# Optimization experiments

Measured on AMD Instinct MI355X. Metric: run time of the kernel, lower is better.

Reference implementation:

```python
import jax, jax.numpy as jnp
import numpy as np

N = 16384
H = 2048
E = 8
I_PER_E = 8192 // E  # expert_intermediate_size = 1024


def setup_inputs() -> dict:
    key = jax.random.key(0)
    k1, k2, k3, k4 = jax.random.split(key, 4)
    hidden_states = jax.random.normal(k1, (N, H), dtype=jnp.float32)
    # sort_idx is a permutation of [0, N): tokens sorted by expert assignment
    sort_idx = jax.random.permutation(k2, N).astype(jnp.int64)
    # kaiming_uniform_ with a=sqrt(5): bound = sqrt(6/((1+a^2)*fan_in)) = 1/sqrt(fan_in)
    bound = 1.0 / np.sqrt(H)
    gate_up_proj = jax.random.uniform(k3, (E, H, 2 * I_PER_E), dtype=jnp.float32,
                                      minval=-bound, maxval=bound)
    # original inits down_proj to zeros; use small random so backward is non-trivial
    down_proj = jax.random.normal(k4, (E, I_PER_E, H), dtype=jnp.float32) * 0.02
    return {"hidden_states": hidden_states, "sort_idx": sort_idx,
            "gate_up_proj": gate_up_proj, "down_proj": down_proj}


def reference(hidden_states, sort_idx, gate_up_proj, down_proj):
    n, h = hidden_states.shape
    e = gate_up_proj.shape[0]
    chunk = n // e
    # gather tokens into expert order: [E, chunk, H]
    sorted_x = hidden_states[sort_idx].reshape(e, chunk, h)
    # fused gate+up grouped GEMM: [E, chunk, 2*I/E]
    gu = jnp.einsum('ech,ehf->ecf', sorted_x, gate_up_proj)
    gate, up = jnp.split(gu, 2, axis=-1)
    activated = jax.nn.silu(gate) * up  # [E, chunk, I/E]
    sorted_out = jnp.einsum('eci,eih->ech', activated, down_proj).reshape(n, h)
    # scatter back: out[sort_idx] = sorted_out
    out = jnp.zeros((n, h), dtype=sorted_out.dtype).at[sort_idx].set(sorted_out)
    return out
```

## Files before the change

### kernel.cpp

```cpp
#include <hip/hip_runtime.h>
#include <hip/hip_bf16.h>

#define N_TOK 16384
#define H_DIM 2048
#define NE 8
#define CHUNK 2048
#define IPE 1024
#define F2 2048

typedef __bf16 bf16;
typedef bf16 bf16x8 __attribute__((ext_vector_type(8)));
typedef float f32x4 __attribute__((ext_vector_type(4)));

typedef __attribute__((address_space(1))) void gvoid;
typedef __attribute__((address_space(3))) void svoid;

__device__ __forceinline__ void gload_lds16(const void* g, void* l) {
  __builtin_amdgcn_global_load_lds((gvoid*)g, (svoid*)l, 16, 0, 0);
}
__device__ __forceinline__ f32x4 MF(bf16x8 a, bf16x8 b, f32x4 c) {
  return __builtin_amdgcn_mfma_f32_16x16x32_bf16(a, b, c, 0, 0, 0);
}

#define BAR() __builtin_amdgcn_s_barrier()
#define LGKM0() asm volatile("s_waitcnt lgkmcnt(0)" ::: "memory")
#define LGKM8() asm volatile("s_waitcnt lgkmcnt(8)" ::: "memory")
#define VM6() asm volatile("s_waitcnt vmcnt(6)" ::: "memory")
#define VM0() asm volatile("s_waitcnt vmcnt(0)" ::: "memory")
#define PRIO(x) __builtin_amdgcn_s_setprio(x)
#define SCHED0() __builtin_amdgcn_sched_barrier(0)

__global__ __launch_bounds__(256) void k_gather(
    const float* __restrict__ x, const int* __restrict__ sidx,
    bf16* __restrict__ xs) {
  int row = blockIdx.x;
  int src = sidx[row];
  const float4* ip = (const float4*)(x + (size_t)src * H_DIM);
  int t = threadIdx.x;
  float4 f0 = ip[t * 2], f1 = ip[t * 2 + 1];
  bf16x8 v;
  v[0] = (bf16)f0.x; v[1] = (bf16)f0.y; v[2] = (bf16)f0.z; v[3] = (bf16)f0.w;
  v[4] = (bf16)f1.x; v[5] = (bf16)f1.y; v[6] = (bf16)f1.z; v[7] = (bf16)f1.w;
  *(bf16x8*)(xs + (size_t)row * H_DIM + t * 8) = v;
}

__global__ __launch_bounds__(256) void k_tr_w1(const float* __restrict__ in,
                                               bf16* __restrict__ out) {
  int e = blockIdx.z;
  int fB = blockIdx.x;
  int hB = blockIdx.y;
  __shared__ bf16 lds[64][68];
  int tx = threadIdx.x & 63;
  int ty = threadIdx.x >> 6;
  const float* ip = in + ((size_t)e * H_DIM + hB * 64) * F2;
  int scol = (tx < 32) ? (fB * 32 + tx) : (1024 + fB * 32 + (tx - 32));
#pragma unroll
  for (int p = 0; p < 16; ++p) {
    int hl = p * 4 + ty;
    lds[hl][tx] = (bf16)ip[(size_t)hl * F2 + scol];
  }
  __syncthreads();
  bf16* op = out + ((size_t)e * F2 + fB * 64) * H_DIM + hB * 64;
#pragma unroll
  for (int p = 0; p < 16; ++p) {
    int fl = p * 4 + ty;
    int g = fl >> 4, w = fl & 15;
    int lcol = ((g >> 1) << 4) + w + ((g & 1) << 5);
    op[(size_t)fl * H_DIM + tx] = lds[tx][lcol];
  }
}

__global__ __launch_bounds__(256) void k_tr_w2(const float* __restrict__ in,
                                               bf16* __restrict__ out) {
  int e = blockIdx.z;
  int hB = blockIdx.x;
  int iB = blockIdx.y;
  __shared__ bf16 lds[64][68];
  int tx = threadIdx.x & 63;
  int ty = threadIdx.x >> 6;
  const float* ip = in + (size_t)e * IPE * H_DIM + (size_t)iB * 64 * H_DIM + hB * 64;
#pragma unroll
  for (int p = 0; p < 16; ++p) {
    int il = p * 4 + ty;
    lds[il][tx] = (bf16)ip[(size_t)il * H_DIM + tx];
  }
  __syncthreads();
  bf16* op = out + (size_t)e * H_DIM * IPE + (size_t)hB * 64 * IPE + iB * 64;
#pragma unroll
  for (int p = 0; p < 16; ++p) {
    int hl = p * 4 + ty;
    op[(size_t)hl * IPE + tx] = lds[tx][hl];
  }
}

template <int KDIM, bool SILU>
__global__ __launch_bounds__(512, 2) void k_gemm8(
    const bf16* __restrict__ Aptr, const bf16* __restrict__ Bptr,
    const int* __restrict__ sidx, bf16* __restrict__ act,
    float* __restrict__ fout) {
  extern __shared__ char smem[];
  const int tid = threadIdx.x, lane = tid & 63, wv = tid >> 6;
  const int wm = wv >> 2, wn = wv & 3;
  constexpr int NT = KDIM / 64;

  int swzwg = (blockIdx.x & 7) * (gridDim.x >> 3) + (blockIdx.x >> 3);
  const int e = swzwg >> 6, bm = (swzwg >> 3) & 7, bn = swzwg & 7;

  const char* Ab = (const char*)(Aptr + ((size_t)e * CHUNK + bm * 256) * KDIM);
  const char* Bb = (const char*)(Bptr + ((size_t)e * 2048 + bn * 256) * KDIM);

  const int L0 = wv * 1024 + lane * 16;
  const int lin0 = L0 ^ (((L0 >> 7) & 7) << 4);
  const int srow0 = lin0 >> 7, scolb = lin0 & 127;

  const int rA = lane & 15;
  const int swzr = (rA & 7) << 4;
  const int cb = (lane >> 4) * 16;

  f32x4 acc[8][4] = {};

  auto stage = [&](int buf, int mat, int half, int kt) {
    const char* gb = (mat == 0) ? Ab : Bb;
    char* ld = smem + buf * 65536 + mat * 32768 + half * 16384 + wv * 1024;
    size_t rb = (size_t)(half * 128 + srow0) * (KDIM * 2) + (size_t)kt * 128 + scolb;
    gload_lds16(gb + rb, ld);
    gload_lds16(gb + rb + (size_t)64 * (KDIM * 2), ld + 8192);
  };
  auto ldA = [&](int buf, int mi, int ks) {
    int lin = ((mi * 16 + rA) << 7) + ks * 64 + cb;
    return *(const bf16x8*)(smem + buf * 65536 + wm * 16384 + (lin ^ swzr));
  };
  auto ldB = [&](int buf, int ni, int ks) {
    int lin = (((wn & 1) * 64 + ni * 16 + rA) << 7) + ks * 64 + cb;
    return *(const bf16x8*)(smem + buf * 65536 + 32768 + (wn >> 1) * 16384 + (lin ^ swzr));
  };

  stage(0, 1, 0, 0); stage(0, 1, 1, 0); stage(0, 0, 0, 0); stage(0, 0, 1, 0);
  stage(1, 1, 0, 1); stage(1, 1, 1, 1); stage(1, 0, 0, 1);
  VM6();
  BAR();

  auto ktile = [&](int t, int cur) {
    const int nxt = cur ^ 1;
    bf16x8 AA[4][2], B0[2][2], B1[2][2];
#pragma unroll
    for (int mi = 0; mi < 4; ++mi) {
      AA[mi][0] = ldA(cur, mi, 0);
      AA[mi][1] = ldA(cur, mi, 1);
    }
#pragma unroll
    for (int ni = 0; ni < 2; ++ni) {
      B0[ni][0] = ldB(cur, ni, 0);
      B0[ni][1] = ldB(cur, ni, 1);
    }
    if (t + 1 < NT) stage(nxt, 0, 1, t + 1);
    LGKM8();
    BAR();
    LGKM0();
    SCHED0();
    PRIO(1);
#pragma unroll
    for (int mi = 0; mi < 4; ++mi)
#pragma unroll
      for (int ni = 0; ni < 2; ++ni) {
        acc[mi][ni] = MF(AA[mi][0], B0[ni][0], acc[mi][ni]);
        acc[mi][ni] = MF(AA[mi][1], B0[ni][1], acc[mi][ni]);
      }
    PRIO(0);
    BAR();
#pragma unroll
    for (int ni = 0; ni < 2; ++ni) {
      B1[ni][0] = ldB(cur, 2 + ni, 0);
      B1[ni][1] = ldB(cur, 2 + ni, 1);
    }
    if (t + 2 < NT) stage(cur, 1, 0, t + 2);
    BAR();
    LGKM0();
    SCHED0();
    PRIO(1);
#pragma unroll
    for (int mi = 0; mi < 4; ++mi)
#pragma unroll
      for (int ni = 0; ni < 2; ++ni) {
        acc[mi][2 + ni] = MF(AA[mi][0], B1[ni][0], acc[mi][2 + ni]);
        acc[mi][2 + ni] = MF(AA[mi][1], B1[ni][1], acc[mi][2 + ni]);
      }
    PRIO(0);
    BAR();
#pragma unroll
    for (int mi = 0; mi < 4; ++mi) {
      AA[mi][0] = ldA(cur, 4 + mi, 0);
      AA[mi][1] = ldA(cur, 4 + mi, 1);
    }
    if (t + 2 < NT) stage(cur, 1, 1, t + 2);
    BAR();
    LGKM0();
    SCHED0();
    PRIO(1);
#pragma unroll
    for (int mi = 0; mi < 4; ++mi)
#pragma unroll
      for (int ni = 0; ni < 2; ++ni) {
        acc[4 + mi][ni] = MF(AA[mi][0], B0[ni][0], acc[4 + mi][ni]);
        acc[4 + mi][ni] = MF(AA[mi][1], B0[ni][1], acc[4 + mi][ni]);
      }
    PRIO(0);
    BAR();
    if (t + 2 < NT) {
      stage(cur, 0, 0, t + 2);
      VM6();
    } else if (t + 1 < NT) {
      VM0();
    }
    BAR();
    PRIO(1);
#pragma unroll
    for (int mi = 0; mi < 4; ++mi)
#pragma unroll
      for (int ni = 0; ni < 2; ++ni) {
        acc[4 + mi][2 + ni] = MF(AA[mi][0], B1[ni][0], acc[4 + mi][2 + ni]);
        acc[4 + mi][2 + ni] = MF(AA[mi][1], B1[ni][1], acc[4 + mi][2 + ni]);
      }
    PRIO(0);
    BAR();
  };

  for (int tt = 0; tt < NT; tt += 2) {
    ktile(tt, 0);
    ktile(tt + 1, 1);
  }

  if constexpr (SILU) {
    bf16* actp = act + ((size_t)e * CHUNK + bm * 256 + wm * 128) * IPE;
    const int r0 = (lane >> 4) * 4;
    const int c0 = bn * 128 + wn * 32 + (lane & 15);
#pragma unroll
    for (int mi = 0; mi < 8; ++mi)
#pragma unroll
      for (int p = 0; p < 2; ++p) {
        f32x4 g = acc[mi][2 * p], u = acc[mi][2 * p + 1];
#pragma unroll
        for (int r = 0; r < 4; ++r) {
          float gv = g[r];
          float a = gv / (1.f + __expf(-gv)) * u[r];
          actp[(size_t)(mi * 16 + r0 + r) * IPE + c0 + p * 16] = (bf16)a;
        }
      }
  } else {
    const int* sp = sidx + e * CHUNK + bm * 256 + wm * 128;
    const int r0 = (lane >> 4) * 4;
    const int c0 = bn * 256 + wn * 64 + (lane & 15);
#pragma unroll
    for (int mi = 0; mi < 8; ++mi)
#pragma unroll
      for (int r = 0; r < 4; ++r) {
        int dst = sp[mi * 16 + r0 + r];
        float* op = fout + (size_t)dst * H_DIM + c0;
#pragma unroll
        for (int ni = 0; ni < 4; ++ni) op[ni * 16] = acc[mi][ni][r];
      }
  }
}

extern "C" void kernel_launch(void* const* d_in, const int* in_sizes, int n_in,
                              void* d_out, int out_size, void* d_ws, size_t ws_size,
                              hipStream_t stream) {
  const float* hidden = (const float*)d_in[0];
  const int* sidx = (const int*)d_in[1];
  const float* w1 = (const float*)d_in[2];
  const float* w2 = (const float*)d_in[3];
  float* out = (float*)d_out;

  char* ws = (char*)d_ws;
  bf16* xs  = (bf16*)(ws);
  bf16* w1t = (bf16*)(ws + (size_t)67108864);
  bf16* act = (bf16*)(ws + (size_t)134217728);
  bf16* w2t = (bf16*)(ws);

  hipFuncSetAttribute((const void*)k_gemm8<H_DIM, true>,
                      hipFuncAttributeMaxDynamicSharedMemorySize, 131072);
  hipFuncSetAttribute((const void*)k_gemm8<IPE, false>,
                      hipFuncAttributeMaxDynamicSharedMemorySize, 131072);

  k_gather<<<dim3(N_TOK), 256, 0, stream>>>(hidden, sidx, xs);
  k_tr_w1<<<dim3(32, 32, NE), 256, 0, stream>>>(w1, w1t);
  k_gemm8<H_DIM, true><<<dim3(512), 512, 131072, stream>>>(xs, w1t, nullptr, act, nullptr);
  k_tr_w2<<<dim3(32, 16, NE), 256, 0, stream>>>(w2, w2t);
  k_gemm8<IPE, false><<<dim3(512), 512, 131072, stream>>>(act, w2t, sidx, nullptr, out);
}
```

Before: 307.0 us.

## Fuse gather and weight transpose/convert into GEMM prologue loads

Removes the separate gather, w1 transpose and w2 transpose kernels. The first GEMM now reads fp32 hidden rows through sort_idx and fp32 w1 columns directly, converts them to bf16 in registers, and writes them into swizzled LDS. The second GEMM does the same for w2. This drops three launches and the workspace round-trips, at the cost of strided scalar fp32 weight loads, more register pressure, and a weaker software pipeline with a full vmcnt(0) wait each tile. The weight conversion is also repeated by every block that shares a weight tile, instead of being done once.

Result: slower. 1.172 ms (+281.9%).

```diff
diff --git a/kernel.cpp b/kernel.cpp
--- a/kernel.cpp
+++ b/kernel.cpp
@@ -25,106 +25,71 @@
 #define BAR() __builtin_amdgcn_s_barrier()
 #define LGKM0() asm volatile("s_waitcnt lgkmcnt(0)" ::: "memory")
 #define LGKM8() asm volatile("s_waitcnt lgkmcnt(8)" ::: "memory")
-#define VM6() asm volatile("s_waitcnt vmcnt(6)" ::: "memory")
 #define VM0() asm volatile("s_waitcnt vmcnt(0)" ::: "memory")
 #define PRIO(x) __builtin_amdgcn_s_setprio(x)
 #define SCHED0() __builtin_amdgcn_sched_barrier(0)
 
-__global__ __launch_bounds__(256) void k_gather(
-    const float* __restrict__ x, const int* __restrict__ sidx,
-    bf16* __restrict__ xs) {
-  int row = blockIdx.x;
-  int src = sidx[row];
-  const float4* ip = (const float4*)(x + (size_t)src * H_DIM);
-  int t = threadIdx.x;
-  float4 f0 = ip[t * 2], f1 = ip[t * 2 + 1];
-  bf16x8 v;
-  v[0] = (bf16)f0.x; v[1] = (bf16)f0.y; v[2] = (bf16)f0.z; v[3] = (bf16)f0.w;
-  v[4] = (bf16)f1.x; v[5] = (bf16)f1.y; v[6] = (bf16)f1.z; v[7] = (bf16)f1.w;
-  *(bf16x8*)(xs + (size_t)row * H_DIM + t * 8) = v;
-}
-
-__global__ __launch_bounds__(256) void k_tr_w1(const float* __restrict__ in,
-                                               bf16* __restrict__ out) {
-  int e = blockIdx.z;
-  int fB = blockIdx.x;
-  int hB = blockIdx.y;
-  __shared__ bf16 lds[64][68];
-  int tx = threadIdx.x & 63;
-  int ty = threadIdx.x >> 6;
-  const float* ip = in + ((size_t)e * H_DIM + hB * 64) * F2;
-  int scol = (tx < 32) ? (fB * 32 + tx) : (1024 + fB * 32 + (tx - 32));
-#pragma unroll
-  for (int p = 0; p < 16; ++p) {
-    int hl = p * 4 + ty;
-    lds[hl][tx] = (bf16)ip[(size_t)hl * F2 + scol];
-  }
-  __syncthreads();
-  bf16* op = out + ((size_t)e * F2 + fB * 64) * H_DIM + hB * 64;
-#pragma unroll
-  for (int p = 0; p < 16; ++p) {
-    int fl = p * 4 + ty;
-    int g = fl >> 4, w = fl & 15;
-    int lcol = ((g >> 1) << 4) + w + ((g & 1) << 5);
-    op[(size_t)fl * H_DIM + tx] = lds[tx][lcol];
-  }
-}
-
-__global__ __launch_bounds__(256) void k_tr_w2(const float* __restrict__ in,
-                                               bf16* __restrict__ out) {
-  int e = blockIdx.z;
-  int hB = blockIdx.x;
-  int iB = blockIdx.y;
-  __shared__ bf16 lds[64][68];
-  int tx = threadIdx.x & 63;
-  int ty = threadIdx.x >> 6;
-  const float* ip = in + (size_t)e * IPE * H_DIM + (size_t)iB * 64 * H_DIM + hB * 64;
-#pragma unroll
-  for (int p = 0; p < 16; ++p) {
-    int il = p * 4 + ty;
-    lds[il][tx] = (bf16)ip[(size_t)il * H_DIM + tx];
-  }
-  __syncthreads();
-  bf16* op = out + (size_t)e * H_DIM * IPE + (size_t)hB * 64 * IPE + iB * 64;
-#pragma unroll
-  for (int p = 0; p < 16; ++p) {
-    int hl = p * 4 + ty;
-    op[(size_t)hl * IPE + tx] = lds[tx][hl];
-  }
-}
-
-template <int KDIM, bool SILU>
-__global__ __launch_bounds__(512, 2) void k_gemm8(
-    const bf16* __restrict__ Aptr, const bf16* __restrict__ Bptr,
-    const int* __restrict__ sidx, bf16* __restrict__ act,
-    float* __restrict__ fout) {
+__global__ __launch_bounds__(512, 2) void k_mlp1(
+    const float* __restrict__ hidden, const int* __restrict__ sidx,
+    const float* __restrict__ w1, bf16* __restrict__ act) {
   extern __shared__ char smem[];
   const int tid = threadIdx.x, lane = tid & 63, wv = tid >> 6;
   const int wm = wv >> 2, wn = wv & 3;
-  constexpr int NT = KDIM / 64;
-
-  int swzwg = (blockIdx.x & 7) * (gridDim.x >> 3) + (blockIdx.x >> 3);
-  const int e = swzwg >> 6, bm = (swzwg >> 3) & 7, bn = swzwg & 7;
-
-  const char* Ab = (const char*)(Aptr + ((size_t)e * CHUNK + bm * 256) * KDIM);
-  const char* Bb = (const char*)(Bptr + ((size_t)e * 2048 + bn * 256) * KDIM);
-
-  const int L0 = wv * 1024 + lane * 16;
-  const int lin0 = L0 ^ (((L0 >> 7) & 7) << 4);
-  const int srow0 = lin0 >> 7, scolb = lin0 & 127;
+  constexpr int NT = H_DIM / 64;
+
+  const int orig = blockIdx.x;
+  const int e = orig >> 6, bm = (orig >> 3) & 7, bn = orig & 7;
+
+  const int mA = tid >> 1;
+  const int khalf = (tid & 1) * 32;
+  const int srcTok = sidx[e * CHUNK + bm * 256 + mA];
+  const float* Arow = hidden + (size_t)srcTok * H_DIM + khalf;
+  const int AwOff = ((mA >> 7) << 14) + ((mA & 127) << 7);
+  const int swzA = (mA & 7) << 4;
+
+  const int np = tid >> 1;
+  const int fcol = bn * 128 + ((np >> 6) & 3) * 32 + ((np >> 5) & 1) * 16 +
+                   (np & 15) + ((np >> 4) & 1) * 1024;
+  const float* Bcol = w1 + (size_t)e * H_DIM * F2 + fcol;
+  const int BwOff = 32768 + ((np >> 7) << 14) + ((np & 127) << 7);
+  const int swzB = (np & 7) << 4;
 
   const int rA = lane & 15;
   const int swzr = (rA & 7) << 4;
   const int cb = (lane >> 4) * 16;
 
   f32x4 acc[8][4] = {};
-
-  auto stage = [&](int buf, int mat, int half, int kt) {
-    const char* gb = (mat == 0) ? Ab : Bb;
-    char* ld = smem + buf * 65536 + mat * 32768 + half * 16384 + wv * 1024;
-    size_t rb = (size_t)(half * 128 + srow0) * (KDIM * 2) + (size_t)kt * 128 + scolb;
-    gload_lds16(gb + rb, ld);
-    gload_lds16(gb + rb + (size_t)64 * (KDIM * 2), ld + 8192);
+  float4 aload[8];
+  float bl[32];
+
+  auto issueA = [&](int kbase) {
+#pragma unroll
+    for (int j = 0; j < 8; ++j)
+      aload[j] = *(const float4*)(Arow + kbase + j * 4);
+  };
+  auto writeA = [&](int buf) {
+#pragma unroll
+    for (int w = 0; w < 4; ++w) {
+      float4 u0 = aload[2 * w], u1 = aload[2 * w + 1];
+      bf16x8 tv;
+      tv[0] = (bf16)u0.x; tv[1] = (bf16)u0.y; tv[2] = (bf16)u0.z; tv[3] = (bf16)u0.w;
+      tv[4] = (bf16)u1.x; tv[5] = (bf16)u1.y; tv[6] = (bf16)u1.z; tv[7] = (bf16)u1.w;
+      *(bf16x8*)(smem + buf * 65536 + AwOff + ((khalf * 2 + w * 16) ^ swzA)) = tv;
+    }
+  };
+  auto issueB = [&](int kbase) {
+    const float* bp = Bcol + (size_t)(kbase + khalf) * F2;
+#pragma unroll
+    for (int j = 0; j < 32; ++j) bl[j] = bp[(size_t)j * F2];
+  };
+  auto writeB = [&](int buf) {
+#pragma unroll
+    for (int w = 0; w < 4; ++w) {
+      bf16x8 tv;
+#pragma unroll
+      for (int i = 0; i < 8; ++i) tv[i] = (bf16)bl[w * 8 + i];
+      *(bf16x8*)(smem + buf * 65536 + BwOff + ((khalf * 2 + w * 16) ^ swzB)) = tv;
+    }
   };
   auto ldA = [&](int buf, int mi, int ks) {
     int lin = ((mi * 16 + rA) << 7) + ks * 64 + cb;
@@ -135,9 +100,12 @@
     return *(const bf16x8*)(smem + buf * 65536 + 32768 + (wn >> 1) * 16384 + (lin ^ swzr));
   };
 
-  stage(0, 1, 0, 0); stage(0, 1, 1, 0); stage(0, 0, 0, 0); stage(0, 0, 1, 0);
-  stage(1, 1, 0, 1); stage(1, 1, 1, 1); stage(1, 0, 0, 1);
-  VM6();
+  issueA(0);
+  issueB(0);
+  writeA(0);
+  writeB(0);
+  issueA(64);
+  LGKM0();
   BAR();
 
   auto ktile = [&](int t, int cur) {
@@ -153,7 +121,6 @@
       B0[ni][0] = ldB(cur, ni, 0);
       B0[ni][1] = ldB(cur, ni, 1);
     }
-    if (t + 1 < NT) stage(nxt, 0, 1, t + 1);
     LGKM8();
     BAR();
     LGKM0();
@@ -173,7 +140,7 @@
       B1[ni][0] = ldB(cur, 2 + ni, 0);
       B1[ni][1] = ldB(cur, 2 + ni, 1);
     }
-    if (t + 2 < NT) stage(cur, 1, 0, t + 2);
+    if (t + 1 < NT) writeA(nxt);
     BAR();
     LGKM0();
     SCHED0();
@@ -192,7 +159,7 @@
       AA[mi][0] = ldA(cur, 4 + mi, 0);
       AA[mi][1] = ldA(cur, 4 + mi, 1);
     }
-    if (t + 2 < NT) stage(cur, 1, 1, t + 2);
+    if (t + 1 < NT) issueB((t + 1) * 64);
     BAR();
     LGKM0();
     SCHED0();
@@ -206,12 +173,9 @@
       }
     PRIO(0);
     BAR();
-    if (t + 2 < NT) {
-      stage(cur, 0, 0, t + 2);
-      VM6();
-    } else if (t + 1 < NT) {
-      VM0();
-    }
+    if (t + 1 < NT) writeB(nxt);
+    if (t + 2 < NT) issueA((t + 2) * 64);
+    LGKM0();
     BAR();
     PRIO(1);
 #pragma unroll
@@ -230,36 +194,192 @@
     ktile(tt + 1, 1);
   }
 
-  if constexpr (SILU) {
-    bf16* actp = act + ((size_t)e * CHUNK + bm * 256 + wm * 128) * IPE;
-    const int r0 = (lane >> 4) * 4;
-    const int c0 = bn * 128 + wn * 32 + (lane & 15);
-#pragma unroll
-    for (int mi = 0; mi < 8; ++mi)
-#pragma unroll
-      for (int p = 0; p < 2; ++p) {
-        f32x4 g = acc[mi][2 * p], u = acc[mi][2 * p + 1];
-#pragma unroll
-        for (int r = 0; r < 4; ++r) {
-          float gv = g[r];
-          float a = gv / (1.f + __expf(-gv)) * u[r];
-          actp[(size_t)(mi * 16 + r0 + r) * IPE + c0 + p * 16] = (bf16)a;
-        }
-      }
-  } else {
-    const int* sp = sidx + e * CHUNK + bm * 256 + wm * 128;
-    const int r0 = (lane >> 4) * 4;
-    const int c0 = bn * 256 + wn * 64 + (lane & 15);
-#pragma unroll
-    for (int mi = 0; mi < 8; ++mi)
+  bf16* actp = act + ((size_t)e * CHUNK + bm * 256 + wm * 128) * IPE;
+  const int r0 = (lane >> 4) * 4;
+  const int c0 = bn * 128 + wn * 32 + (lane & 15);
+#pragma unroll
+  for (int mi = 0; mi < 8; ++mi)
+#pragma unroll
+    for (int p = 0; p < 2; ++p) {
+      f32x4 g = acc[mi][2 * p], u = acc[mi][2 * p + 1];
 #pragma unroll
       for (int r = 0; r < 4; ++r) {
-        int dst = sp[mi * 16 + r0 + r];
-        float* op = fout + (size_t)dst * H_DIM + c0;
-#pragma unroll
-        for (int ni = 0; ni < 4; ++ni) op[ni * 16] = acc[mi][ni][r];
-      }
+        float gv = g[r];
+        float a = gv / (1.f + __expf(-gv)) * u[r];
+        actp[(size_t)(mi * 16 + r0 + r) * IPE + c0 + p * 16] = (bf16)a;
+      }
+    }
+}
+
+__global__ __launch_bounds__(512, 2) void k_mlp2(
+    const bf16* __restrict__ act, const float* __restrict__ w2,
+    const int* __restrict__ sidx, float* __restrict__ out) {
+  extern __shared__ char smem[];
+  const int tid = threadIdx.x, lane = tid & 63, wv = tid >> 6;
+  const int wm = wv >> 2, wn = wv & 3;
+  constexpr int NT = IPE / 64;
+
+  const int orig = blockIdx.x;
+  const int e = orig >> 6, bm = (orig >> 3) & 7, bn = orig & 7;
+
+  const char* Ab = (const char*)(act + ((size_t)e * CHUNK + bm * 256) * IPE);
+
+  const int L0 = wv * 1024 + lane * 16;
+  const int lin0 = L0 ^ (((L0 >> 7) & 7) << 4);
+  const int srow0 = lin0 >> 7, scolb = lin0 & 127;
+
+  const int np = tid >> 1;
+  const int khalf = (tid & 1) * 32;
+  const float* Bcol = w2 + (size_t)e * IPE * H_DIM + bn * 256 + np;
+  const int BwOff = 32768 + ((np >> 7) << 14) + ((np & 127) << 7);
+  const int swzB = (np & 7) << 4;
+
+  const int rA = lane & 15;
+  const int swzr = (rA & 7) << 4;
+  const int cb = (lane >> 4) * 16;
+
+  f32x4 acc[8][4] = {};
+  float bl[32];
+
+  auto stageA = [&](int buf, int kt) {
+#pragma unroll
+    for (int half = 0; half < 2; ++half) {
+      char* ld = smem + buf * 65536 + half * 16384 + wv * 1024;
+      size_t rb = (size_t)(half * 128 + srow0) * (IPE * 2) + (size_t)kt * 128 + scolb;
+      gload_lds16(Ab + rb, ld);
+      gload_lds16(Ab + rb + (size_t)64 * (IPE * 2), ld + 8192);
+    }
+  };
+  auto issueB = [&](int kbase) {
+    const float* bp = Bcol + (size_t)(kbase + khalf) * H_DIM;
+#pragma unroll
+    for (int j = 0; j < 32; ++j) bl[j] = bp[(size_t)j * H_DIM];
+  };
+  auto writeB = [&](int buf) {
+#pragma unroll
+    for (int w = 0; w < 4; ++w) {
+      bf16x8 tv;
+#pragma unroll
+      for (int i = 0; i < 8; ++i) tv[i] = (bf16)bl[w * 8 + i];
+      *(bf16x8*)(smem + buf * 65536 + BwOff + ((khalf * 2 + w * 16) ^ swzB)) = tv;
+    }
+  };
+  auto ldA = [&](int buf, int mi, int ks) {
+    int lin = ((mi * 16 + rA) << 7) + ks * 64 + cb;
+    return *(const bf16x8*)(smem + buf * 65536 + wm * 16384 + (lin ^ swzr));
+  };
+  auto ldB = [&](int buf, int ni, int ks) {
+    int lin = (((wn & 1) * 64 + ni * 16 + rA) << 7) + ks * 64 + cb;
+    return *(const bf16x8*)(smem + buf * 65536 + 32768 + (wn >> 1) * 16384 + (lin ^ swzr));
+  };
+
+  stageA(0, 0);
+  issueB(0);
+  writeB(0);
+  VM0();
+  LGKM0();
+  BAR();
+
+  auto ktile = [&](int t, int cur) {
+    const int nxt = cur ^ 1;
+    bf16x8 AA[4][2], B0[2][2], B1[2][2];
+#pragma unroll
+    for (int mi = 0; mi < 4; ++mi) {
+      AA[mi][0] = ldA(cur, mi, 0);
+      AA[mi][1] = ldA(cur, mi, 1);
+    }
+#pragma unroll
+    for (int ni = 0; ni < 2; ++ni) {
+      B0[ni][0] = ldB(cur, ni, 0);
+      B0[ni][1] = ldB(cur, ni, 1);
+    }
+    if (t + 1 < NT) stageA(nxt, t + 1);
+    LGKM8();
+    BAR();
+    LGKM0();
+    SCHED0();
+    PRIO(1);
+#pragma unroll
+    for (int mi = 0; mi < 4; ++mi)
+#pragma unroll
+      for (int ni = 0; ni < 2; ++ni) {
+        acc[mi][ni] = MF(AA[mi][0], B0[ni][0], acc[mi][ni]);
+        acc[mi][ni] = MF(AA[mi][1], B0[ni][1], acc[mi][ni]);
+      }
+    PRIO(0);
+    BAR();
+#pragma unroll
+    for (int ni = 0; ni < 2; ++ni) {
+      B1[ni][0] = ldB(cur, 2 + ni, 0);
+      B1[ni][1] = ldB(cur, 2 + ni, 1);
+    }
+    BAR();
+    LGKM0();
+    SCHED0();
+    PRIO(1);
+#pragma unroll
+    for (int mi = 0; mi < 4; ++mi)
+#pragma unroll
+      for (int ni = 0; ni < 2; ++ni) {
+        acc[mi][2 + ni] = MF(AA[mi][0], B1[ni][0], acc[mi][2 + ni]);
+        acc[mi][2 + ni] = MF(AA[mi][1], B1[ni][1], acc[mi][2 + ni]);
+      }
+    PRIO(0);
+    BAR();
+#pragma unroll
+    for (int mi = 0; mi < 4; ++mi) {
+      AA[mi][0] = ldA(cur, 4 + mi, 0);
+      AA[mi][1] = ldA(cur, 4 + mi, 1);
+    }
+    if (t + 1 < NT) issueB((t + 1) * 64);
+    BAR();
+    LGKM0();
+    SCHED0();
+    PRIO(1);
+#pragma unroll
+    for (int mi = 0; mi < 4; ++mi)
+#pragma unroll
+      for (int ni = 0; ni < 2; ++ni) {
+        acc[4 + mi][ni] = MF(AA[mi][0], B0[ni][0], acc[4 + mi][ni]);
+        acc[4 + mi][ni] = MF(AA[mi][1], B0[ni][1], acc[4 + mi][ni]);
+      }
+    PRIO(0);
+    BAR();
+    if (t + 1 < NT) {
+      writeB(nxt);
+      VM0();
+    }
+    LGKM0();
+    BAR();
+    PRIO(1);
+#pragma unroll
+    for (int mi = 0; mi < 4; ++mi)
+#pragma unroll
+      for (int ni = 0; ni < 2; ++ni) {
+        acc[4 + mi][2 + ni] = MF(AA[mi][0], B1[ni][0], acc[4 + mi][2 + ni]);
+        acc[4 + mi][2 + ni] = MF(AA[mi][1], B1[ni][1], acc[4 + mi][2 + ni]);
+      }
+    PRIO(0);
+    BAR();
+  };
+
+  for (int tt = 0; tt < NT; tt += 2) {
+    ktile(tt, 0);
+    ktile(tt + 1, 1);
   }
+
+  const int* sp = sidx + e * CHUNK + bm * 256 + wm * 128;
+  const int r0 = (lane >> 4) * 4;
+  const int c0 = bn * 256 + wn * 64 + (lane & 15);
+#pragma unroll
+  for (int mi = 0; mi < 8; ++mi)
+#pragma unroll
+    for (int r = 0; r < 4; ++r) {
+      int dst = sp[mi * 16 + r0 + r];
+      float* op = out + (size_t)dst * H_DIM + c0;
+#pragma unroll
+      for (int ni = 0; ni < 4; ++ni) op[ni * 16] = acc[mi][ni][r];
+    }
 }
 
 extern "C" void kernel_launch(void* const* d_in, const int* in_sizes, int n_in,
@@ -271,20 +391,13 @@
   const float* w2 = (const float*)d_in[3];
   float* out = (float*)d_out;
 
-  char* ws = (char*)d_ws;
-  bf16* xs  = (bf16*)(ws);
-  bf16* w1t = (bf16*)(ws + (size_t)67108864);
-  bf16* act = (bf16*)(ws + (size_t)134217728);
-  bf16* w2t = (bf16*)(ws);
-
-  hipFuncSetAttribute((const void*)k_gemm8<H_DIM, true>,
+  bf16* act = (bf16*)d_ws;
+
+  hipFuncSetAttribute((const void*)k_mlp1,
                       hipFuncAttributeMaxDynamicSharedMemorySize, 131072);
-  hipFuncSetAttribute((const void*)k_gemm8<IPE, false>,
+  hipFuncSetAttribute((const void*)k_mlp2,
                       hipFuncAttributeMaxDynamicSharedMemorySize, 131072);
 
-  k_gather<<<dim3(N_TOK), 256, 0, stream>>>(hidden, sidx, xs);
-  k_tr_w1<<<dim3(32, 32, NE), 256, 0, stream>>>(w1, w1t);
-  k_gemm8<H_DIM, true><<<dim3(512), 512, 131072, stream>>>(xs, w1t, nullptr, act, nullptr);
-  k_tr_w2<<<dim3(32, 16, NE), 256, 0, stream>>>(w2, w2t);
-  k_gemm8<IPE, false><<<dim3(512), 512, 131072, stream>>>(act, w2t, sidx, nullptr, out);
+  k_mlp1<<<dim3(512), 512, 131072, stream>>>(hidden, sidx, w1, act);
+  k_mlp2<<<dim3(512), 512, 131072, stream>>>(act, w2, sidx, out);
 }
```

## Fuse token gather and bf16 cast into first grouped GEMM A-loads

Applied to the files above, without the earlier changes.

Removes the separate gather kernel that wrote a bf16 sorted copy of the hidden states. The first GEMM now reads fp32 rows through sort_idx in registers, converts them to bf16 and writes them into swizzled LDS, with the global loads software-pipelined inside the k-tile loop. The weight transpose kernels are also changed to write 16 contiguous bf16 values per thread as vector stores instead of scalar stores. The cost is that the GEMM reads twice the A bytes in fp32 through a register path instead of direct-to-LDS loads, which adds register pressure and VALU conversion work in the main loop.

Result: slower. 425.6 us (+38.6%).

```diff
diff --git a/kernel.cpp b/kernel.cpp
--- a/kernel.cpp
+++ b/kernel.cpp
@@ -29,20 +29,6 @@
 #define VM0() asm volatile("s_waitcnt vmcnt(0)" ::: "memory")
 #define PRIO(x) __builtin_amdgcn_s_setprio(x)
 #define SCHED0() __builtin_amdgcn_sched_barrier(0)
-
-__global__ __launch_bounds__(256) void k_gather(
-    const float* __restrict__ x, const int* __restrict__ sidx,
-    bf16* __restrict__ xs) {
-  int row = blockIdx.x;
-  int src = sidx[row];
-  const float4* ip = (const float4*)(x + (size_t)src * H_DIM);
-  int t = threadIdx.x;
-  float4 f0 = ip[t * 2], f1 = ip[t * 2 + 1];
-  bf16x8 v;
-  v[0] = (bf16)f0.x; v[1] = (bf16)f0.y; v[2] = (bf16)f0.z; v[3] = (bf16)f0.w;
-  v[4] = (bf16)f1.x; v[5] = (bf16)f1.y; v[6] = (bf16)f1.z; v[7] = (bf16)f1.w;
-  *(bf16x8*)(xs + (size_t)row * H_DIM + t * 8) = v;
-}
 
 __global__ __launch_bounds__(256) void k_tr_w1(const float* __restrict__ in,
                                                bf16* __restrict__ out) {
@@ -60,14 +46,15 @@
     lds[hl][tx] = (bf16)ip[(size_t)hl * F2 + scol];
   }
   __syncthreads();
-  bf16* op = out + ((size_t)e * F2 + fB * 64) * H_DIM + hB * 64;
-#pragma unroll
-  for (int p = 0; p < 16; ++p) {
-    int fl = p * 4 + ty;
-    int g = fl >> 4, w = fl & 15;
-    int lcol = ((g >> 1) << 4) + w + ((g & 1) << 5);
-    op[(size_t)fl * H_DIM + tx] = lds[tx][lcol];
-  }
+  int fl = threadIdx.x >> 2, hseg = (threadIdx.x & 3) * 16;
+  int g = fl >> 4, w = fl & 15;
+  int lcol = ((g >> 1) << 4) + w + ((g & 1) << 5);
+  bf16 v[16];
+#pragma unroll
+  for (int j = 0; j < 16; ++j) v[j] = lds[hseg + j][lcol];
+  bf16* op = out + ((size_t)e * F2 + fB * 64 + fl) * H_DIM + hB * 64 + hseg;
+  *(bf16x8*)op = *(bf16x8*)&v[0];
+  *(bf16x8*)(op + 8) = *(bf16x8*)&v[8];
 }
 
 __global__ __launch_bounds__(256) void k_tr_w2(const float* __restrict__ in,
@@ -85,22 +72,210 @@
     lds[il][tx] = (bf16)ip[(size_t)il * H_DIM + tx];
   }
   __syncthreads();
-  bf16* op = out + (size_t)e * H_DIM * IPE + (size_t)hB * 64 * IPE + iB * 64;
-#pragma unroll
-  for (int p = 0; p < 16; ++p) {
-    int hl = p * 4 + ty;
-    op[(size_t)hl * IPE + tx] = lds[tx][hl];
-  }
-}
-
-template <int KDIM, bool SILU>
-__global__ __launch_bounds__(512, 2) void k_gemm8(
-    const bf16* __restrict__ Aptr, const bf16* __restrict__ Bptr,
-    const int* __restrict__ sidx, bf16* __restrict__ act,
-    float* __restrict__ fout) {
+  int hl = threadIdx.x >> 2, iseg = (threadIdx.x & 3) * 16;
+  bf16 v[16];
+#pragma unroll
+  for (int j = 0; j < 16; ++j) v[j] = lds[iseg + j][hl];
+  bf16* op = out + ((size_t)e * H_DIM + hB * 64 + hl) * IPE + iB * 64 + iseg;
+  *(bf16x8*)op = *(bf16x8*)&v[0];
+  *(bf16x8*)(op + 8) = *(bf16x8*)&v[8];
+}
+
+__global__ __launch_bounds__(512, 2) void k_gemm1f(
+    const float* __restrict__ hidden, const int* __restrict__ sidx,
+    const bf16* __restrict__ W, bf16* __restrict__ act) {
   extern __shared__ char smem[];
   const int tid = threadIdx.x, lane = tid & 63, wv = tid >> 6;
   const int wm = wv >> 2, wn = wv & 3;
+  constexpr int KDIM = H_DIM;
+  constexpr int NT = KDIM / 64;
+
+  int swzwg = (blockIdx.x & 7) * (gridDim.x >> 3) + (blockIdx.x >> 3);
+  const int e = swzwg >> 6, bm = (swzwg >> 3) & 7, bn = swzwg & 7;
+
+  const char* Bb = (const char*)(W + ((size_t)e * F2 + bn * 256) * KDIM);
+
+  const int L0 = wv * 1024 + lane * 16;
+  const int lin0 = L0 ^ (((L0 >> 7) & 7) << 4);
+  const int srow0 = lin0 >> 7, scolb = lin0 & 127;
+
+  const int arow_loc = tid >> 3;
+  const int k0 = (tid & 7) * 8;
+  const float* Arow[4];
+  int AwOff[4];
+#pragma unroll
+  for (int p = 0; p < 4; ++p) {
+    int row = p * 64 + arow_loc;
+    int tok = sidx[e * CHUNK + bm * 256 + row];
+    Arow[p] = hidden + (size_t)tok * H_DIM + k0;
+    AwOff[p] = (row >> 7) * 16384 + ((row & 127) << 7) + ((k0 * 2) ^ ((row & 7) << 4));
+  }
+
+  const int rA = lane & 15;
+  const int swzr = (rA & 7) << 4;
+  const int cb = (lane >> 4) * 16;
+
+  f32x4 acc[8][4] = {};
+  float4 al[4];
+
+  auto issueB = [&](int buf, int kt) {
+#pragma unroll
+    for (int half = 0; half < 2; ++half) {
+      char* ld = smem + buf * 65536 + 32768 + half * 16384 + wv * 1024;
+      size_t rb = (size_t)(half * 128 + srow0) * (KDIM * 2) + (size_t)kt * 128 + scolb;
+      gload_lds16(Bb + rb, ld);
+      gload_lds16(Bb + rb + (size_t)64 * (KDIM * 2), ld + 8192);
+    }
+  };
+  auto issueA = [&](int h, int kt) {
+#pragma unroll
+    for (int q = 0; q < 2; ++q) {
+      const float* s = Arow[h * 2 + q] + kt * 64;
+      al[q * 2] = *(const float4*)s;
+      al[q * 2 + 1] = *(const float4*)(s + 4);
+    }
+  };
+  auto writeA = [&](int buf, int h) {
+#pragma unroll
+    for (int q = 0; q < 2; ++q) {
+      float4 u0 = al[q * 2], u1 = al[q * 2 + 1];
+      bf16x8 tv;
+      tv[0] = (bf16)u0.x; tv[1] = (bf16)u0.y; tv[2] = (bf16)u0.z; tv[3] = (bf16)u0.w;
+      tv[4] = (bf16)u1.x; tv[5] = (bf16)u1.y; tv[6] = (bf16)u1.z; tv[7] = (bf16)u1.w;
+      *(bf16x8*)(smem + buf * 65536 + AwOff[h * 2 + q]) = tv;
+    }
+  };
+  auto ldA = [&](int buf, int mi, int ks) {
+    int lin = ((mi * 16 + rA) << 7) + ks * 64 + cb;
+    return *(const bf16x8*)(smem + buf * 65536 + wm * 16384 + (lin ^ swzr));
+  };
+  auto ldB = [&](int buf, int ni, int ks) {
+    int lin = (((wn & 1) * 64 + ni * 16 + rA) << 7) + ks * 64 + cb;
+    return *(const bf16x8*)(smem + buf * 65536 + 32768 + (wn >> 1) * 16384 + (lin ^ swzr));
+  };
+
+  issueB(0, 0);
+  issueB(1, 1);
+  issueA(0, 0);
+  writeA(0, 0);
+  issueA(1, 0);
+  writeA(0, 1);
+  LGKM0();
+  BAR();
+
+  auto ktile = [&](int t, int cur) {
+    const int nxt = cur ^ 1;
+    bf16x8 AA[4][2], B0[2][2], B1[2][2];
+    if (t + 1 < NT) issueA(0, t + 1);
+#pragma unroll
+    for (int mi = 0; mi < 4; ++mi) {
+      AA[mi][0] = ldA(cur, mi, 0);
+      AA[mi][1] = ldA(cur, mi, 1);
+    }
+#pragma unroll
+    for (int ni = 0; ni < 2; ++ni) {
+      B0[ni][0] = ldB(cur, ni, 0);
+      B0[ni][1] = ldB(cur, ni, 1);
+    }
+    LGKM8();
+    BAR();
+    LGKM0();
+    SCHED0();
+    PRIO(1);
+#pragma unroll
+    for (int mi = 0; mi < 4; ++mi)
+#pragma unroll
+      for (int ni = 0; ni < 2; ++ni) {
+        acc[mi][ni] = MF(AA[mi][0], B0[ni][0], acc[mi][ni]);
+        acc[mi][ni] = MF(AA[mi][1], B0[ni][1], acc[mi][ni]);
+      }
+    PRIO(0);
+    BAR();
+#pragma unroll
+    for (int ni = 0; ni < 2; ++ni) {
+      B1[ni][0] = ldB(cur, 2 + ni, 0);
+      B1[ni][1] = ldB(cur, 2 + ni, 1);
+    }
+    BAR();
+    LGKM0();
+    SCHED0();
+    PRIO(1);
+#pragma unroll
+    for (int mi = 0; mi < 4; ++mi)
+#pragma unroll
+      for (int ni = 0; ni < 2; ++ni) {
+        acc[mi][2 + ni] = MF(AA[mi][0], B1[ni][0], acc[mi][2 + ni]);
+        acc[mi][2 + ni] = MF(AA[mi][1], B1[ni][1], acc[mi][2 + ni]);
+      }
+    PRIO(0);
+    BAR();
+#pragma unroll
+    for (int mi = 0; mi < 4; ++mi) {
+      AA[mi][0] = ldA(cur, 4 + mi, 0);
+      AA[mi][1] = ldA(cur, 4 + mi, 1);
+    }
+    if (t + 1 < NT) {
+      writeA(nxt, 0);
+      issueA(1, t + 1);
+    }
+    BAR();
+    LGKM0();
+    SCHED0();
+    PRIO(1);
+#pragma unroll
+    for (int mi = 0; mi < 4; ++mi)
+#pragma unroll
+      for (int ni = 0; ni < 2; ++ni) {
+        acc[4 + mi][ni] = MF(AA[mi][0], B0[ni][0], acc[4 + mi][ni]);
+        acc[4 + mi][ni] = MF(AA[mi][1], B0[ni][1], acc[4 + mi][ni]);
+      }
+    PRIO(0);
+    BAR();
+    if (t + 1 < NT) writeA(nxt, 1);
+    if (t + 2 < NT) issueB(cur, t + 2);
+    LGKM0();
+    BAR();
+    PRIO(1);
+#pragma unroll
+    for (int mi = 0; mi < 4; ++mi)
+#pragma unroll
+      for (int ni = 0; ni < 2; ++ni) {
+        acc[4 + mi][2 + ni] = MF(AA[mi][0], B1[ni][0], acc[4 + mi][2 + ni]);
+        acc[4 + mi][2 + ni] = MF(AA[mi][1], B1[ni][1], acc[4 + mi][2 + ni]);
+      }
+    PRIO(0);
+    BAR();
+  };
+
+  for (int tt = 0; tt < NT; tt += 2) {
+    ktile(tt, 0);
+    ktile(tt + 1, 1);
+  }
+
+  bf16* actp = act + ((size_t)e * CHUNK + bm * 256 + wm * 128) * IPE;
+  const int r0 = (lane >> 4) * 4;
+  const int c0 = bn * 128 + wn * 32 + (lane & 15);
+#pragma unroll
+  for (int mi = 0; mi < 8; ++mi)
+#pragma unroll
+    for (int p = 0; p < 2; ++p) {
+      f32x4 g = acc[mi][2 * p], u = acc[mi][2 * p + 1];
+#pragma unroll
+      for (int r = 0; r < 4; ++r) {
+        float gv = g[r];
+        float a = gv / (1.f + __expf(-gv)) * u[r];
+        actp[(size_t)(mi * 16 + r0 + r) * IPE + c0 + p * 16] = (bf16)a;
+      }
+    }
+}
+
+__global__ __launch_bounds__(512, 2) void k_gemm2(
+    const bf16* __restrict__ Aptr, const bf16* __restrict__ Bptr,
+    const int* __restrict__ sidx, float* __restrict__ fout) {
+  extern __shared__ char smem[];
+  const int tid = threadIdx.x, lane = tid & 63, wv = tid >> 6;
+  const int wm = wv >> 2, wn = wv & 3;
+  constexpr int KDIM = IPE;
   constexpr int NT = KDIM / 64;
 
   int swzwg = (blockIdx.x & 7) * (gridDim.x >> 3) + (blockIdx.x >> 3);
@@ -230,36 +405,18 @@
     ktile(tt + 1, 1);
   }
 
-  if constexpr (SILU) {
-    bf16* actp = act + ((size_t)e * CHUNK + bm * 256 + wm * 128) * IPE;
-    const int r0 = (lane >> 4) * 4;
-    const int c0 = bn * 128 + wn * 32 + (lane & 15);
-#pragma unroll
-    for (int mi = 0; mi < 8; ++mi)
-#pragma unroll
-      for (int p = 0; p < 2; ++p) {
-        f32x4 g = acc[mi][2 * p], u = acc[mi][2 * p + 1];
-#pragma unroll
-        for (int r = 0; r < 4; ++r) {
-          float gv = g[r];
-          float a = gv / (1.f + __expf(-gv)) * u[r];
-          actp[(size_t)(mi * 16 + r0 + r) * IPE + c0 + p * 16] = (bf16)a;
-        }
-      }
-  } else {
-    const int* sp = sidx + e * CHUNK + bm * 256 + wm * 128;
-    const int r0 = (lane >> 4) * 4;
-    const int c0 = bn * 256 + wn * 64 + (lane & 15);
-#pragma unroll
-    for (int mi = 0; mi < 8; ++mi)
-#pragma unroll
-      for (int r = 0; r < 4; ++r) {
-        int dst = sp[mi * 16 + r0 + r];
-        float* op = fout + (size_t)dst * H_DIM + c0;
-#pragma unroll
-        for (int ni = 0; ni < 4; ++ni) op[ni * 16] = acc[mi][ni][r];
-      }
-  }
+  const int* sp = sidx + e * CHUNK + bm * 256 + wm * 128;
+  const int r0 = (lane >> 4) * 4;
+  const int c0 = bn * 256 + wn * 64 + (lane & 15);
+#pragma unroll
+  for (int mi = 0; mi < 8; ++mi)
+#pragma unroll
+    for (int r = 0; r < 4; ++r) {
+      int dst = sp[mi * 16 + r0 + r];
+      float* op = fout + (size_t)dst * H_DIM + c0;
+#pragma unroll
+      for (int ni = 0; ni < 4; ++ni) op[ni * 16] = acc[mi][ni][r];
+    }
 }
 
 extern "C" void kernel_launch(void* const* d_in, const int* in_sizes, int n_in,
@@ -272,19 +429,17 @@
   float* out = (float*)d_out;
 
   char* ws = (char*)d_ws;
-  bf16* xs  = (bf16*)(ws);
-  bf16* w1t = (bf16*)(ws + (size_t)67108864);
-  bf16* act = (bf16*)(ws + (size_t)134217728);
-  bf16* w2t = (bf16*)(ws);
-
-  hipFuncSetAttribute((const void*)k_gemm8<H_DIM, true>,
+  bf16* w1t = (bf16*)(ws);
+  bf16* w2t = (bf16*)(ws + (size_t)67108864);
+  bf16* act = (bf16*)(ws + (size_t)100663296);
+
+  hipFuncSetAttribute((const void*)k_gemm1f,
                       hipFuncAttributeMaxDynamicSharedMemorySize, 131072);
-  hipFuncSetAttribute((const void*)k_gemm8<IPE, false>,
+  hipFuncSetAttribute((const void*)k_gemm2,
                       hipFuncAttributeMaxDynamicSharedMemorySize, 131072);
 
-  k_gather<<<dim3(N_TOK), 256, 0, stream>>>(hidden, sidx, xs);
   k_tr_w1<<<dim3(32, 32, NE), 256, 0, stream>>>(w1, w1t);
-  k_gemm8<H_DIM, true><<<dim3(512), 512, 131072, stream>>>(xs, w1t, nullptr, act, nullptr);
   k_tr_w2<<<dim3(32, 16, NE), 256, 0, stream>>>(w2, w2t);
-  k_gemm8<IPE, false><<<dim3(512), 512, 131072, stream>>>(act, w2t, sidx, nullptr, out);
-}
+  k_gemm1f<<<dim3(512), 512, 131072, stream>>>(hidden, sidx, w1t, act);
+  k_gemm2<<<dim3(512), 512, 131072, stream>>>(act, w2t, sidx, out);
+}
```

## Fuse gather and weight transposes into one prep kernel with vectorized access

Applied to the files above, without the earlier changes.

Merges the token gather/convert kernel and both weight transpose kernels into a single launch that dispatches on block index. The transposes now use float4 global loads and 16-byte bf16 stores instead of scalar accesses. The workspace layout changes so w2t no longer aliases xs and gets its own region, with act moved after it. This removes two launches and the serialization gap between the first GEMM and the w2 transpose, and widens memory transactions. In exchange it uses more workspace and puts all preprocessing before the first GEMM.

New measurement: 302.3 us. About the same (-1.5%).

```diff
diff --git a/kernel.cpp b/kernel.cpp
--- a/kernel.cpp
+++ b/kernel.cpp
@@ -30,66 +30,67 @@
 #define PRIO(x) __builtin_amdgcn_s_setprio(x)
 #define SCHED0() __builtin_amdgcn_sched_barrier(0)
 
-__global__ __launch_bounds__(256) void k_gather(
-    const float* __restrict__ x, const int* __restrict__ sidx,
-    bf16* __restrict__ xs) {
-  int row = blockIdx.x;
-  int src = sidx[row];
-  const float4* ip = (const float4*)(x + (size_t)src * H_DIM);
-  int t = threadIdx.x;
-  float4 f0 = ip[t * 2], f1 = ip[t * 2 + 1];
-  bf16x8 v;
-  v[0] = (bf16)f0.x; v[1] = (bf16)f0.y; v[2] = (bf16)f0.z; v[3] = (bf16)f0.w;
-  v[4] = (bf16)f1.x; v[5] = (bf16)f1.y; v[6] = (bf16)f1.z; v[7] = (bf16)f1.w;
-  *(bf16x8*)(xs + (size_t)row * H_DIM + t * 8) = v;
-}
-
-__global__ __launch_bounds__(256) void k_tr_w1(const float* __restrict__ in,
-                                               bf16* __restrict__ out) {
-  int e = blockIdx.z;
-  int fB = blockIdx.x;
-  int hB = blockIdx.y;
+__global__ __launch_bounds__(256) void k_prep(
+    const float* __restrict__ hidden, const int* __restrict__ sidx,
+    const float* __restrict__ w1, const float* __restrict__ w2,
+    bf16* __restrict__ xs, bf16* __restrict__ w1t, bf16* __restrict__ w2t) {
+  int b = blockIdx.x;
+  int tid = threadIdx.x;
+  if (b < 16384) {
+    int row = b;
+    int src = sidx[row];
+    const float4* ip = (const float4*)(hidden + (size_t)src * H_DIM);
+    float4 f0 = ip[tid * 2], f1 = ip[tid * 2 + 1];
+    bf16x8 v;
+    v[0] = (bf16)f0.x; v[1] = (bf16)f0.y; v[2] = (bf16)f0.z; v[3] = (bf16)f0.w;
+    v[4] = (bf16)f1.x; v[5] = (bf16)f1.y; v[6] = (bf16)f1.z; v[7] = (bf16)f1.w;
+    *(bf16x8*)(xs + (size_t)row * H_DIM + tid * 8) = v;
+    return;
+  }
   __shared__ bf16 lds[64][68];
-  int tx = threadIdx.x & 63;
-  int ty = threadIdx.x >> 6;
-  const float* ip = in + ((size_t)e * H_DIM + hB * 64) * F2;
-  int scol = (tx < 32) ? (fB * 32 + tx) : (1024 + fB * 32 + (tx - 32));
-#pragma unroll
-  for (int p = 0; p < 16; ++p) {
-    int hl = p * 4 + ty;
-    lds[hl][tx] = (bf16)ip[(size_t)hl * F2 + scol];
-  }
-  __syncthreads();
-  bf16* op = out + ((size_t)e * F2 + fB * 64) * H_DIM + hB * 64;
-#pragma unroll
-  for (int p = 0; p < 16; ++p) {
-    int fl = p * 4 + ty;
+  if (b < 24576) {
+    int i1 = b - 16384;
+    int fB = i1 & 31, hB = (i1 >> 5) & 31, e = i1 >> 10;
+    const float* ip = w1 + ((size_t)e * H_DIM + hB * 64) * F2;
+#pragma unroll
+    for (int p = 0; p < 4; ++p) {
+      int idx = p * 256 + tid;
+      int half = idx >> 9, rem = idx & 511;
+      int row = rem >> 3, c4 = rem & 7;
+      float4 v = *(const float4*)(ip + (size_t)row * F2 + half * 1024 + fB * 32 + c4 * 4);
+      bf16* d = &lds[row][half * 32 + c4 * 4];
+      d[0] = (bf16)v.x; d[1] = (bf16)v.y; d[2] = (bf16)v.z; d[3] = (bf16)v.w;
+    }
+    __syncthreads();
+    int fl = tid >> 2, hseg = (tid & 3) * 16;
     int g = fl >> 4, w = fl & 15;
     int lcol = ((g >> 1) << 4) + w + ((g & 1) << 5);
-    op[(size_t)fl * H_DIM + tx] = lds[tx][lcol];
-  }
-}
-
-__global__ __launch_bounds__(256) void k_tr_w2(const float* __restrict__ in,
-                                               bf16* __restrict__ out) {
-  int e = blockIdx.z;
-  int hB = blockIdx.x;
-  int iB = blockIdx.y;
-  __shared__ bf16 lds[64][68];
-  int tx = threadIdx.x & 63;
-  int ty = threadIdx.x >> 6;
-  const float* ip = in + (size_t)e * IPE * H_DIM + (size_t)iB * 64 * H_DIM + hB * 64;
-#pragma unroll
-  for (int p = 0; p < 16; ++p) {
-    int il = p * 4 + ty;
-    lds[il][tx] = (bf16)ip[(size_t)il * H_DIM + tx];
-  }
-  __syncthreads();
-  bf16* op = out + (size_t)e * H_DIM * IPE + (size_t)hB * 64 * IPE + iB * 64;
-#pragma unroll
-  for (int p = 0; p < 16; ++p) {
-    int hl = p * 4 + ty;
-    op[(size_t)hl * IPE + tx] = lds[tx][hl];
+    bf16 v[16];
+#pragma unroll
+    for (int j = 0; j < 16; ++j) v[j] = lds[hseg + j][lcol];
+    bf16* op = w1t + ((size_t)e * F2 + fB * 64 + fl) * H_DIM + hB * 64 + hseg;
+    *(bf16x8*)op = *(bf16x8*)&v[0];
+    *(bf16x8*)(op + 8) = *(bf16x8*)&v[8];
+  } else {
+    int i2 = b - 24576;
+    int hB = i2 & 31, iB = (i2 >> 5) & 15, e = i2 >> 9;
+    const float* ip = w2 + (size_t)e * IPE * H_DIM + (size_t)iB * 64 * H_DIM + hB * 64;
+#pragma unroll
+    for (int p = 0; p < 4; ++p) {
+      int idx = p * 256 + tid;
+      int row = idx >> 4, c4 = idx & 15;
+      float4 v = *(const float4*)(ip + (size_t)row * H_DIM + c4 * 4);
+      bf16* d = &lds[row][c4 * 4];
+      d[0] = (bf16)v.x; d[1] = (bf16)v.y; d[2] = (bf16)v.z; d[3] = (bf16)v.w;
+    }
+    __syncthreads();
+    int hl = tid >> 2, iseg = (tid & 3) * 16;
+    bf16 v[16];
+#pragma unroll
+    for (int j = 0; j < 16; ++j) v[j] = lds[iseg + j][hl];
+    bf16* op = w2t + ((size_t)e * H_DIM + hB * 64 + hl) * IPE + iB * 64 + iseg;
+    *(bf16x8*)op = *(bf16x8*)&v[0];
+    *(bf16x8*)(op + 8) = *(bf16x8*)&v[8];
   }
 }
 
@@ -274,17 +275,15 @@
   char* ws = (char*)d_ws;
   bf16* xs  = (bf16*)(ws);
   bf16* w1t = (bf16*)(ws + (size_t)67108864);
-  bf16* act = (bf16*)(ws + (size_t)134217728);
-  bf16* w2t = (bf16*)(ws);
+  bf16* w2t = (bf16*)(ws + (size_t)134217728);
+  bf16* act = (bf16*)(ws + (size_t)167772160);
 
   hipFuncSetAttribute((const void*)k_gemm8<H_DIM, true>,
                       hipFuncAttributeMaxDynamicSharedMemorySize, 131072);
   hipFuncSetAttribute((const void*)k_gemm8<IPE, false>,
                       hipFuncAttributeMaxDynamicSharedMemorySize, 131072);
 
-  k_gather<<<dim3(N_TOK), 256, 0, stream>>>(hidden, sidx, xs);
-  k_tr_w1<<<dim3(32, 32, NE), 256, 0, stream>>>(w1, w1t);
+  k_prep<<<dim3(28672), 256, 0, stream>>>(hidden, sidx, w1, w2, xs, w1t, w2t);
   k_gemm8<H_DIM, true><<<dim3(512), 512, 131072, stream>>>(xs, w1t, nullptr, act, nullptr);
-  k_tr_w2<<<dim3(32, 16, NE), 256, 0, stream>>>(w2, w2t);
   k_gemm8<IPE, false><<<dim3(512), 512, 131072, stream>>>(act, w2t, sidx, nullptr, out);
 }
```
